# Kernel optimization log

Measured on AMD Instinct MI355X. Metric: run time of the kernel, lower is better.

## Reference

```python
import jax, jax.numpy as jnp
import numpy as np

N_NODES = 50000
N_EDGES = 500000
D = 128  # node/edge feature dim


def setup_inputs() -> dict:
    key = jax.random.key(0)
    k1, k2, k3, k4, k5 = jax.random.split(key, 5)
    x_node = jax.random.normal(k1, (N_NODES, D), dtype=jnp.float32)
    x_edge = jax.random.normal(k2, (N_EDGES, D), dtype=jnp.float32)
    edge_index = jax.random.randint(k3, (N_EDGES, 2), 0, N_NODES, dtype=jnp.int64)
    # MLP params: Linear(3D -> D) -> ReLU -> Linear(D -> D)
    W1 = jax.random.normal(k4, (3 * D, D), dtype=jnp.float32) * (1.0 / np.sqrt(3 * D))
    b1 = jnp.zeros((D,), dtype=jnp.float32)
    W2 = jax.random.normal(k5, (D, D), dtype=jnp.float32) * (1.0 / np.sqrt(D))
    b2 = jnp.zeros((D,), dtype=jnp.float32)
    return {"x_node": x_node, "x_edge": x_edge, "edge_index": edge_index,
            "W1": W1, "b1": b1, "W2": W2, "b2": b2}


def reference(x_node, x_edge, edge_index, W1, b1, W2, b2):
    # gather node features at both endpoints of each edge
    v0 = x_node[edge_index[:, 0]]          # [E, D]
    v1 = x_node[edge_index[:, 1]]          # [E, D]
    x_new = jnp.concatenate([v0, v1, x_edge], axis=1)  # [E, 3D]
    h = jax.nn.relu(x_new @ W1 + b1)       # [E, D]
    x_edge_new = h @ W2 + b2               # [E, D]
    return x_edge_new
```

## Files before the change

### kernel.cpp

```cpp
#include <hip/hip_runtime.h>
#include <stdint.h>

#define D 128
#define MT 32
#define XS 392
#define HS 136

typedef short short8 __attribute__((ext_vector_type(8)));
typedef float f32x16 __attribute__((ext_vector_type(16)));

__device__ __forceinline__ unsigned short f2bf(float f) {
    union { float f; uint32_t u; } v;
    v.f = f;
    uint32_t u = v.u;
    uint32_t r = (u + 0x7fffu + ((u >> 16) & 1u)) >> 16;
    return (unsigned short)r;
}

__global__ void pack_weights_kernel(const float* __restrict__ W1,
                                    const float* __restrict__ W2,
                                    unsigned short* __restrict__ W1p,
                                    unsigned short* __restrict__ W2p) {
    int t = blockIdx.x * 256 + threadIdx.x;
    if (t < 6144) {
        int kt = t >> 8, nt = (t >> 6) & 3, lane = t & 63;
        int n = nt * 32 + (lane & 31);
        int kb = kt * 16 + (lane >> 5) * 8;
        unsigned short* dst = W1p + t * 8;
        #pragma unroll
        for (int j = 0; j < 8; ++j) dst[j] = f2bf(W1[(kb + j) * D + n]);
    } else if (t < 8192) {
        int u = t - 6144;
        int kt = u >> 8, nt = (u >> 6) & 3, lane = u & 63;
        int n = nt * 32 + (lane & 31);
        int kb = kt * 16 + (lane >> 5) * 8;
        unsigned short* dst = W2p + u * 8;
        #pragma unroll
        for (int j = 0; j < 8; ++j) dst[j] = f2bf(W2[(kb + j) * D + n]);
    }
}

__global__ __launch_bounds__(256, 6) void edge_mlp_kernel(
    const float* __restrict__ x_node,
    const float* __restrict__ x_edge,
    const int* __restrict__ eidx,
    const unsigned short* __restrict__ W1p,
    const unsigned short* __restrict__ W2p,
    const float* __restrict__ b1,
    const float* __restrict__ b2,
    float* __restrict__ out,
    int E) {
    __shared__ unsigned short lds[MT * XS];
    unsigned short* Hs = lds;

    const int t = threadIdx.x;
    const int r0 = blockIdx.x * MT;

    {
        const int lane32 = t & 31;
        const int rsub = t >> 5;

        int rgc[4];
        float4 v2[4];
        #pragma unroll
        for (int rb = 0; rb < 4; ++rb) {
            int rg = r0 + rb * 8 + rsub;
            rgc[rb] = rg < E ? rg : E - 1;
            v2[rb] = ((const float4*)(x_edge + (size_t)rgc[rb] * D))[lane32];
        }
        int2 e[4];
        #pragma unroll
        for (int rb = 0; rb < 4; ++rb)
            e[rb] = ((const int2*)eidx)[rgc[rb]];
        float4 v0[4], v1[4];
        #pragma unroll
        for (int rb = 0; rb < 4; ++rb) {
            v0[rb] = ((const float4*)(x_node + (size_t)e[rb].x * D))[lane32];
            v1[rb] = ((const float4*)(x_node + (size_t)e[rb].y * D))[lane32];
        }
        #pragma unroll
        for (int rb = 0; rb < 4; ++rb) {
            int row = rb * 8 + rsub;
            unsigned short* base = &lds[row * XS + lane32 * 4];
            ushort4 p;
            p.x = f2bf(v0[rb].x); p.y = f2bf(v0[rb].y);
            p.z = f2bf(v0[rb].z); p.w = f2bf(v0[rb].w);
            *(ushort4*)(base) = p;
            p.x = f2bf(v1[rb].x); p.y = f2bf(v1[rb].y);
            p.z = f2bf(v1[rb].z); p.w = f2bf(v1[rb].w);
            *(ushort4*)(base + 128) = p;
            p.x = f2bf(v2[rb].x); p.y = f2bf(v2[rb].y);
            p.z = f2bf(v2[rb].z); p.w = f2bf(v2[rb].w);
            *(ushort4*)(base + 256) = p;
        }
    }
    __syncthreads();

    const int w = t >> 6;
    const int lane = t & 63;
    const int lrow = lane & 31;
    const int khalf = (lane >> 5) * 8;
    const int n = w * 32 + lrow;
    const int rbump = (lane >> 5) * 4;

    f32x16 acc;
    #pragma unroll
    for (int i = 0; i < 16; ++i) acc[i] = 0.f;

    #pragma unroll 8
    for (int kt = 0; kt < 24; ++kt) {
        short8 a = *(const short8*)&lds[lrow * XS + kt * 16 + khalf];
        short8 b = *(const short8*)(W1p + ((kt * 4 + w) * 64 + lane) * 8);
        acc = __builtin_amdgcn_mfma_f32_32x32x16_bf16(a, b, acc, 0, 0, 0);
    }
    __syncthreads();

    {
        float b1v = b1[n];
        #pragma unroll
        for (int r = 0; r < 16; ++r) {
            int rr = (r & 3) + 8 * (r >> 2) + rbump;
            Hs[rr * HS + n] = f2bf(fmaxf(acc[r] + b1v, 0.f));
        }
    }
    __syncthreads();

    f32x16 c;
    #pragma unroll
    for (int i = 0; i < 16; ++i) c[i] = 0.f;

    #pragma unroll
    for (int kt = 0; kt < 8; ++kt) {
        short8 a = *(const short8*)&Hs[lrow * HS + kt * 16 + khalf];
        short8 b = *(const short8*)(W2p + ((kt * 4 + w) * 64 + lane) * 8);
        c = __builtin_amdgcn_mfma_f32_32x32x16_bf16(a, b, c, 0, 0, 0);
    }

    {
        float b2v = b2[n];
        #pragma unroll
        for (int r = 0; r < 16; ++r) {
            int rr = (r & 3) + 8 * (r >> 2) + rbump;
            int rg = r0 + rr;
            if (rg < E) out[(size_t)rg * D + n] = c[r] + b2v;
        }
    }
}

extern "C" void kernel_launch(void* const* d_in, const int* in_sizes, int n_in,
                              void* d_out, int out_size, void* d_ws, size_t ws_size,
                              hipStream_t stream) {
    const float* x_node = (const float*)d_in[0];
    const float* x_edge = (const float*)d_in[1];
    const int*   eidx   = (const int*)d_in[2];
    const float* W1     = (const float*)d_in[3];
    const float* b1     = (const float*)d_in[4];
    const float* W2     = (const float*)d_in[5];
    const float* b2     = (const float*)d_in[6];
    float* out = (float*)d_out;

    const int E = in_sizes[1] / D;

    unsigned short* W1p = (unsigned short*)d_ws;
    unsigned short* W2p = W1p + 6144 * 8;

    pack_weights_kernel<<<32, 256, 0, stream>>>(W1, W2, W1p, W2p);

    int nblk = (E + MT - 1) / MT;
    edge_mlp_kernel<<<nblk, 256, 0, stream>>>(x_node, x_edge, eidx, W1p, W2p, b1, b2, out, E);
}
```

Before: 521.4 us.

## Gather edge inputs directly into LDS via global_load_lds and convert at MFMA time

Replaces the register-staged gather (load fp32, convert to bf16, store to LDS) with asynchronous global_load_lds transfers that put fp32 node and edge rows straight into LDS in MFMA operand layout. The bf16 conversion moves into the first GEMM loop, and the loop is fully unrolled. This avoids VGPR staging and the separate convert/store phase. In exchange, LDS per block roughly doubles, the launch-bounds occupancy hint drops from 6 to 3, and every wave redundantly converts the whole A tile.

```diff
diff --git a/kernel.cpp b/kernel.cpp
--- a/kernel.cpp
+++ b/kernel.cpp
@@ -3,7 +3,6 @@
 
 #define D 128
 #define MT 32
-#define XS 392
 #define HS 136
 
 typedef short short8 __attribute__((ext_vector_type(8)));
@@ -40,7 +39,7 @@
     }
 }
 
-__global__ __launch_bounds__(256, 6) void edge_mlp_kernel(
+__global__ __launch_bounds__(256, 3) void edge_mlp_kernel(
     const float* __restrict__ x_node,
     const float* __restrict__ x_edge,
     const int* __restrict__ eidx,
@@ -50,68 +49,57 @@
     const float* __restrict__ b2,
     float* __restrict__ out,
     int E) {
-    __shared__ unsigned short lds[MT * XS];
-    unsigned short* Hs = lds;
+    __shared__ float Af[12288];
+    unsigned short* Hs = (unsigned short*)Af;
 
     const int t = threadIdx.x;
     const int r0 = blockIdx.x * MT;
 
-    {
-        const int lane32 = t & 31;
-        const int rsub = t >> 5;
+    const int w = t >> 6;
+    const int l = t & 63;
+    const int lrow = l & 31;
+    const int hi = l >> 5;
+    const int khalf = hi * 8;
+    const int n = w * 32 + lrow;
+    const int rbump = hi * 4;
 
-        int rgc[4];
-        float4 v2[4];
-        #pragma unroll
-        for (int rb = 0; rb < 4; ++rb) {
-            int rg = r0 + rb * 8 + rsub;
-            rgc[rb] = rg < E ? rg : E - 1;
-            v2[rb] = ((const float4*)(x_edge + (size_t)rgc[rb] * D))[lane32];
-        }
-        int2 e[4];
-        #pragma unroll
-        for (int rb = 0; rb < 4; ++rb)
-            e[rb] = ((const int2*)eidx)[rgc[rb]];
-        float4 v0[4], v1[4];
-        #pragma unroll
-        for (int rb = 0; rb < 4; ++rb) {
-            v0[rb] = ((const float4*)(x_node + (size_t)e[rb].x * D))[lane32];
-            v1[rb] = ((const float4*)(x_node + (size_t)e[rb].y * D))[lane32];
-        }
-        #pragma unroll
-        for (int rb = 0; rb < 4; ++rb) {
-            int row = rb * 8 + rsub;
-            unsigned short* base = &lds[row * XS + lane32 * 4];
-            ushort4 p;
-            p.x = f2bf(v0[rb].x); p.y = f2bf(v0[rb].y);
-            p.z = f2bf(v0[rb].z); p.w = f2bf(v0[rb].w);
-            *(ushort4*)(base) = p;
-            p.x = f2bf(v1[rb].x); p.y = f2bf(v1[rb].y);
-            p.z = f2bf(v1[rb].z); p.w = f2bf(v1[rb].w);
-            *(ushort4*)(base + 128) = p;
-            p.x = f2bf(v2[rb].x); p.y = f2bf(v2[rb].y);
-            p.z = f2bf(v2[rb].z); p.w = f2bf(v2[rb].w);
-            *(ushort4*)(base + 256) = p;
-        }
+    const int row = r0 + lrow;
+    const int rc = row < E ? row : E - 1;
+    const int2 el = ((const int2*)eidx)[rc];
+    const float* g0 = x_node + (size_t)el.x * D + hi * 8;
+    const float* g1 = x_node + (size_t)el.y * D + hi * 8;
+    const float* g2 = x_edge + (size_t)rc * D + hi * 8;
+
+    #pragma unroll
+    for (int i = 0; i < 6; ++i) {
+        const int kt = w * 6 + i;
+        const float* gb = (kt < 8 ? g0 : (kt < 16 ? g1 : g2)) + (kt & 7) * 16;
+        float* ld = Af + kt * 512;
+        __builtin_amdgcn_global_load_lds(
+            (const __attribute__((address_space(1))) void*)(gb),
+            (__attribute__((address_space(3))) void*)(ld), 16, 0, 0);
+        __builtin_amdgcn_global_load_lds(
+            (const __attribute__((address_space(1))) void*)(gb + 4),
+            (__attribute__((address_space(3))) void*)(ld + 256), 16, 0, 0);
     }
+    asm volatile("s_waitcnt vmcnt(0)" ::: "memory");
     __syncthreads();
-
-    const int w = t >> 6;
-    const int lane = t & 63;
-    const int lrow = lane & 31;
-    const int khalf = (lane >> 5) * 8;
-    const int n = w * 32 + lrow;
-    const int rbump = (lane >> 5) * 4;
 
     f32x16 acc;
     #pragma unroll
     for (int i = 0; i < 16; ++i) acc[i] = 0.f;
 
-    #pragma unroll 8
+    #pragma unroll
     for (int kt = 0; kt < 24; ++kt) {
-        short8 a = *(const short8*)&lds[lrow * XS + kt * 16 + khalf];
-        short8 b = *(const short8*)(W1p + ((kt * 4 + w) * 64 + lane) * 8);
-        acc = __builtin_amdgcn_mfma_f32_32x32x16_bf16(a, b, acc, 0, 0, 0);
+        float4 fa0 = *(const float4*)(Af + kt * 512 + l * 4);
+        float4 fa1 = *(const float4*)(Af + kt * 512 + 256 + l * 4);
+        union { short8 s; ushort4 h[2]; } av;
+        av.h[0].x = f2bf(fa0.x); av.h[0].y = f2bf(fa0.y);
+        av.h[0].z = f2bf(fa0.z); av.h[0].w = f2bf(fa0.w);
+        av.h[1].x = f2bf(fa1.x); av.h[1].y = f2bf(fa1.y);
+        av.h[1].z = f2bf(fa1.z); av.h[1].w = f2bf(fa1.w);
+        short8 b = *(const short8*)(W1p + ((kt * 4 + w) * 64 + l) * 8);
+        acc = __builtin_amdgcn_mfma_f32_32x32x16_bf16(av.s, b, acc, 0, 0, 0);
     }
     __syncthreads();
 
@@ -132,7 +120,7 @@
     #pragma unroll
     for (int kt = 0; kt < 8; ++kt) {
         short8 a = *(const short8*)&Hs[lrow * HS + kt * 16 + khalf];
-        short8 b = *(const short8*)(W2p + ((kt * 4 + w) * 64 + lane) * 8);
+        short8 b = *(const short8*)(W2p + ((kt * 4 + w) * 64 + l) * 8);
         c = __builtin_amdgcn_mfma_f32_32x32x16_bf16(a, b, c, 0, 0, 0);
     }
 
```

Measured after the change: 620.4 us. 19.0% more time.
